# Kernel tuning notes

Measured on AMD Instinct MI355X. Metric: run time of the kernel, lower is better.

Reference implementation:

```python
import jax, jax.numpy as jnp
import numpy as np

S = 2_000_000   # sequence length (tokens/residues)
P = 1_000_000   # number of 'positive' (pu) indices
E = 20          # number of experts / alphabet size


def setup_inputs() -> dict:
    key = jax.random.key(0)
    k1, k2, k3, k4, k5 = jax.random.split(key, 5)
    # x[0, :, :20] acts as per-token one-hot over the 20-letter alphabet;
    # argmax of uniform noise gives a valid routing index per token.
    x = jax.random.uniform(k1, (1, S, E), dtype=jnp.float32)
    h = jax.random.normal(k2, (S, 2), dtype=jnp.float32)        # 'output1' from inner model
    W = jax.random.normal(k3, (E, 2, 2), dtype=jnp.float32) * 0.5  # per-expert Linear weight [out,in]
    b = jax.random.normal(k4, (E, 2), dtype=jnp.float32) * 0.1     # per-expert Linear bias
    # unique, sorted positive indices (torch.index_select semantics)
    pu_index = jnp.sort(jax.random.permutation(k5, S)[:P]).astype(jnp.int32)
    return {"x": x, "h": h, "W": W, "b": b, "pu_index": pu_index}


def reference(x, h, W, b, pu_index):
    # recognize_res: per-token expert index from one-hot channels 0:20 of x[0]
    res_index = jnp.argmax(x[0, :, :E], axis=-1)                 # [S] int
    # verblizer_function: per-token expert Linear(2,2) + Softmax, fused as
    # gather expert params -> batched matmul -> softmax
    Wt = W[res_index]                                            # [S, 2, 2]
    bt = b[res_index]                                            # [S, 2]
    y = jnp.einsum('si,soi->so', h, Wt) + bt                     # torch Linear: h @ W.T + b
    y = jax.nn.softmax(y, axis=-1)                               # output1 after verblizer
    # pu_train: rows at pu_index first (in pu order), remaining rows after
    n_tok = h.shape[0]
    mask = jnp.zeros((n_tok,), dtype=bool).at[pu_index].set(True)
    non = jnp.nonzero(~mask, size=n_tok - pu_index.shape[0])[0]  # preserves original order
    perm = jnp.concatenate([pu_index.astype(non.dtype), non])
    y2 = y[perm]                                                 # output2
    return (y, y2)
```

## Files before the change

### kernel.cpp

```cpp
#include <hip/hip_runtime.h>
#include <math.h>

#define TPB  256
#define TILE 512
#define GRAN 64

typedef float v4f __attribute__((ext_vector_type(4)));
typedef float v2f __attribute__((ext_vector_type(2)));

__global__ __launch_bounds__(TPB) void boundary_kernel(
    const int* __restrict__ pu, int P, int NB, int* __restrict__ boundary)
{
    int i = blockIdx.x * TPB + threadIdx.x;
    if (i >= P) return;
    int cur = pu[i];
    int lo  = (i == 0) ? 0 : (pu[i - 1] / GRAN) + 1;
    int hi  = cur / GRAN;
    for (int bb = lo; bb <= hi; ++bb) boundary[bb] = i;
    if (i == P - 1)
        for (int bb = hi + 1; bb <= NB; ++bb) boundary[bb] = P;
}

__global__ __launch_bounds__(TPB) void verblizer_fused_kernel(
    const v4f*  __restrict__ x4,
    const v2f*  __restrict__ h2,
    const float* __restrict__ W,
    const float* __restrict__ b,
    const int*   __restrict__ pu,
    const int*   __restrict__ boundary,
    v2f*         __restrict__ y,
    v2f*         __restrict__ y2,
    int S, int P)
{
    __shared__ uint2 scratch[(TPB / 64) * 640];

    const int t    = threadIdx.x;
    const int lane = t & 63;
    const int w    = t >> 6;
    const int B0   = min((int)blockIdx.x * TILE, S - TILE);

    const int base = B0 + 128 * w;
    const int s0   = base + lane;
    const int s1   = base + 64 + lane;

    const int wi = __builtin_amdgcn_readfirstlane(base >> 6);
    const int r0 = boundary[wi];
    const int r1 = boundary[wi + 1];
    const int r2 = boundary[wi + 2];

    v4f xv[10];
    const v4f* xp = x4 + (size_t)base * 5;
#pragma unroll
    for (int j = 0; j < 10; ++j)
        xv[j] = __builtin_nontemporal_load(xp + 64 * j + lane);

    const v2f h0 = __builtin_nontemporal_load(h2 + s0);
    const v2f h1 = __builtin_nontemporal_load(h2 + s1);
    const int pA = pu[min(r0 + lane, P - 1)];
    const int pB = pu[min(r1 + lane, P - 1)];

    const int nA = r1 - r0;
    const int nB = r2 - r1;
    unsigned long long mA = (lane < nA) ? (1ull << ((unsigned)(pA - base) & 63)) : 0ull;
    unsigned long long mB = (lane < nB) ? (1ull << ((unsigned)(pB - base - 64) & 63)) : 0ull;
#pragma unroll
    for (int d = 1; d < 64; d <<= 1) {
        mA |= __shfl_xor(mA, d, 64);
        mB |= __shfl_xor(mB, d, 64);
    }
    const unsigned long long lt = (1ull << lane) - 1ull;
    const int  rankA = r0 + __popcll(mA & lt);
    const int  rankB = r1 + __popcll(mB & lt);
    const bool fA    = (mA >> lane) & 1;
    const bool fB    = (mB >> lane) & 1;

    uint2* sw = scratch + w * 640;
#pragma unroll
    for (int j = 0; j < 10; ++j) {
        v4f v = xv[j];
        float best = v.x; int bi = 0;
        if (v.y > best) { best = v.y; bi = 1; }
        if (v.z > best) { best = v.z; bi = 2; }
        if (v.w > best) { best = v.w; bi = 3; }
        const int flat = 64 * j + lane;
        const int c    = flat % 5;
        sw[flat] = make_uint2(__float_as_uint(best), (unsigned)(4 * c + bi));
    }

#pragma unroll
    for (int half = 0; half < 2; ++half) {
        const int   tl   = half ? (64 + lane) : lane;
        const v2f   hv   = half ? h1 : h0;
        const int   s    = half ? s1 : s0;
        const bool  f    = half ? fB : fA;
        const int   rnk  = half ? rankB : rankA;

        float best = -INFINITY; int bi = 0;
#pragma unroll
        for (int c = 0; c < 5; ++c) {
            uint2 p = sw[5 * tl + c];
            float v = __uint_as_float(p.x);
            if (v > best) { best = v; bi = (int)p.y; }
        }

        const float4 wv = *(const float4*)(W + bi * 4);
        const float2 bv = *(const float2*)(b + bi * 2);
        float y0 = fmaf(hv.x, wv.x, fmaf(hv.y, wv.y, bv.x));
        float y1 = fmaf(hv.x, wv.z, fmaf(hv.y, wv.w, bv.y));
        float mx = fmaxf(y0, y1);
        float e0 = __expf(y0 - mx);
        float e1 = __expf(y1 - mx);
        float inv = 1.0f / (e0 + e1);
        v2f yo = { e0 * inv, e1 * inv };

        __builtin_nontemporal_store(yo, y + s);
        const int dst = f ? rnk : (P + s - rnk);
        __builtin_nontemporal_store(yo, y2 + dst);
    }
}

extern "C" void kernel_launch(void* const* d_in, const int* in_sizes, int n_in,
                              void* d_out, int out_size, void* d_ws, size_t ws_size,
                              hipStream_t stream) {
    const float* x  = (const float*)d_in[0];
    const float* h  = (const float*)d_in[1];
    const float* W  = (const float*)d_in[2];
    const float* b  = (const float*)d_in[3];
    const int*   pu = (const int*)d_in[4];

    const int S  = in_sizes[1] / 2;
    const int P  = in_sizes[4];
    const int NB = S / GRAN;

    int* boundary = (int*)d_ws;

    v2f* y  = (v2f*)d_out;
    v2f* y2 = (v2f*)d_out + S;

    boundary_kernel<<<(P + TPB - 1) / TPB, TPB, 0, stream>>>(pu, P, NB, boundary);

    const int grid = (S + TILE - 1) / TILE;
    verblizer_fused_kernel<<<grid, TPB, 0, stream>>>(
        (const v4f*)x, (const v2f*)h, W, b, pu, boundary, y, y2, S, P);
}
```

Baseline: 240.9 us.

## Replace boundary precompute kernel with per-wave 64-ary search over pu

Removes the separate boundary kernel and its workspace array, and instead has each wavefront find its starting rank in pu with a ballot-based 64-way search. The pu entries for the two 64-token sub-tiles are then gathered from a 128-entry window using shuffles. This drops one kernel launch and its global write/read traffic. In exchange every wave performs several dependent rounds of scattered pu loads (about log64(P) rounds), which adds latency inside the main kernel.

```diff
diff --git a/kernel.cpp b/kernel.cpp
--- a/kernel.cpp
+++ b/kernel.cpp
@@ -3,23 +3,9 @@
 
 #define TPB  256
 #define TILE 512
-#define GRAN 64
 
 typedef float v4f __attribute__((ext_vector_type(4)));
 typedef float v2f __attribute__((ext_vector_type(2)));
-
-__global__ __launch_bounds__(TPB) void boundary_kernel(
-    const int* __restrict__ pu, int P, int NB, int* __restrict__ boundary)
-{
-    int i = blockIdx.x * TPB + threadIdx.x;
-    if (i >= P) return;
-    int cur = pu[i];
-    int lo  = (i == 0) ? 0 : (pu[i - 1] / GRAN) + 1;
-    int hi  = cur / GRAN;
-    for (int bb = lo; bb <= hi; ++bb) boundary[bb] = i;
-    if (i == P - 1)
-        for (int bb = hi + 1; bb <= NB; ++bb) boundary[bb] = P;
-}
 
 __global__ __launch_bounds__(TPB) void verblizer_fused_kernel(
     const v4f*  __restrict__ x4,
@@ -27,7 +13,6 @@
     const float* __restrict__ W,
     const float* __restrict__ b,
     const int*   __restrict__ pu,
-    const int*   __restrict__ boundary,
     v2f*         __restrict__ y,
     v2f*         __restrict__ y2,
     int S, int P)
@@ -43,11 +28,6 @@
     const int s0   = base + lane;
     const int s1   = base + 64 + lane;
 
-    const int wi = __builtin_amdgcn_readfirstlane(base >> 6);
-    const int r0 = boundary[wi];
-    const int r1 = boundary[wi + 1];
-    const int r2 = boundary[wi + 2];
-
     v4f xv[10];
     const v4f* xp = x4 + (size_t)base * 5;
 #pragma unroll
@@ -56,23 +36,6 @@
 
     const v2f h0 = __builtin_nontemporal_load(h2 + s0);
     const v2f h1 = __builtin_nontemporal_load(h2 + s1);
-    const int pA = pu[min(r0 + lane, P - 1)];
-    const int pB = pu[min(r1 + lane, P - 1)];
-
-    const int nA = r1 - r0;
-    const int nB = r2 - r1;
-    unsigned long long mA = (lane < nA) ? (1ull << ((unsigned)(pA - base) & 63)) : 0ull;
-    unsigned long long mB = (lane < nB) ? (1ull << ((unsigned)(pB - base - 64) & 63)) : 0ull;
-#pragma unroll
-    for (int d = 1; d < 64; d <<= 1) {
-        mA |= __shfl_xor(mA, d, 64);
-        mB |= __shfl_xor(mB, d, 64);
-    }
-    const unsigned long long lt = (1ull << lane) - 1ull;
-    const int  rankA = r0 + __popcll(mA & lt);
-    const int  rankB = r1 + __popcll(mB & lt);
-    const bool fA    = (mA >> lane) & 1;
-    const bool fB    = (mB >> lane) & 1;
 
     uint2* sw = scratch + w * 640;
 #pragma unroll
@@ -86,6 +49,52 @@
         const int c    = flat % 5;
         sw[flat] = make_uint2(__float_as_uint(best), (unsigned)(4 * c + bi));
     }
+
+    int lo = 0, n = P;
+    while (n > 64) {
+        const int step = (n + 63) >> 6;
+        const int idx  = lo + lane * step;
+        const int v    = (idx < P) ? pu[idx] : 0x7fffffff;
+        const int c    = __popcll(__ballot(v < base));
+        if (c > 0) lo += (c - 1) * step;
+        n = step + 1;
+    }
+    {
+        const int idx = lo + lane;
+        const int v   = (lane < n && idx < P) ? pu[idx] : 0x7fffffff;
+        lo += __popcll(__ballot(v < base));
+    }
+    const int r0 = lo;
+
+    const int  i0  = r0 + lane;
+    const int  i1  = r0 + 64 + lane;
+    const int  q0  = pu[min(i0, P - 1)];
+    const int  q1  = pu[min(i1, P - 1)];
+    const bool ok0 = i0 < P;
+    const bool ok1 = i1 < P;
+
+    const int nA = __popcll(__ballot(ok0 && q0 < base + 64));
+    const int r1 = r0 + nA;
+    const int nB = __popcll(__ballot(ok0 && q0 >= base + 64 && q0 < base + 128))
+                 + __popcll(__ballot(ok1 && q1 < base + 128));
+    const int ssel = nA + lane;
+    const int pBa  = __shfl(q0, ssel & 63, 64);
+    const int pBb  = __shfl(q1, ssel & 63, 64);
+    const int pB   = (ssel < 64) ? pBa : pBb;
+    const int pA   = q0;
+
+    unsigned long long mA = (lane < nA) ? (1ull << ((unsigned)(pA - base) & 63)) : 0ull;
+    unsigned long long mB = (lane < nB) ? (1ull << ((unsigned)(pB - base - 64) & 63)) : 0ull;
+#pragma unroll
+    for (int d = 1; d < 64; d <<= 1) {
+        mA |= __shfl_xor(mA, d, 64);
+        mB |= __shfl_xor(mB, d, 64);
+    }
+    const unsigned long long lt = (1ull << lane) - 1ull;
+    const int  rankA = r0 + __popcll(mA & lt);
+    const int  rankB = r1 + __popcll(mB & lt);
+    const bool fA    = (mA >> lane) & 1;
+    const bool fB    = (mB >> lane) & 1;
 
 #pragma unroll
     for (int half = 0; half < 2; ++half) {
@@ -130,16 +139,13 @@
 
     const int S  = in_sizes[1] / 2;
     const int P  = in_sizes[4];
-    const int NB = S / GRAN;
 
-    int* boundary = (int*)d_ws;
+    (void)d_ws; (void)ws_size; (void)n_in; (void)out_size;
 
     v2f* y  = (v2f*)d_out;
     v2f* y2 = (v2f*)d_out + S;
 
-    boundary_kernel<<<(P + TPB - 1) / TPB, TPB, 0, stream>>>(pu, P, NB, boundary);
-
     const int grid = (S + TILE - 1) / TILE;
     verblizer_fused_kernel<<<grid, TPB, 0, stream>>>(
-        (const v4f*)x, (const v2f*)h, W, b, pu, boundary, y, y2, S, P);
+        (const v4f*)x, (const v2f*)h, W, b, pu, y, y2, S, P);
 }
```

After: 241.6 us. Within noise of the previous version (+0.3%).
